# Kernel optimization log

Measured on AMD Instinct MI355X. Metric: run time of the kernel, lower is better.

The kernel has to match this reference:

```python
import jax, jax.numpy as jnp
import numpy as np

B, S, E = 4096, 64, 64   # batch, num fields, embed_dim
A, H = 256, 4            # atten_dim, num_heads
HD = A // H              # head_dim = 64


def setup_inputs() -> dict:
    key = jax.random.key(0)
    ks = jax.random.split(key, 12)
    s = lambda fan_in: 1.0 / np.sqrt(fan_in)
    return {
        "query": jax.random.normal(ks[0], (B, S, E), jnp.float32),
        "key_": jax.random.normal(ks[1], (B, S, E), jnp.float32),
        "value": jax.random.normal(ks[2], (B, S, E), jnp.float32),
        "Wq": jax.random.normal(ks[3], (E, A), jnp.float32) * s(E),
        "bq": jax.random.normal(ks[4], (A,), jnp.float32) * s(E),
        "Wk": jax.random.normal(ks[5], (E, A), jnp.float32) * s(E),
        "bk": jax.random.normal(ks[6], (A,), jnp.float32) * s(E),
        "Wv": jax.random.normal(ks[7], (E, A), jnp.float32) * s(E),
        "bv": jax.random.normal(ks[8], (A,), jnp.float32) * s(E),
        "Wu": jax.random.normal(ks[9], (E, H), jnp.float32) * s(E),
        "bu": jax.random.normal(ks[10], (H,), jnp.float32) * s(E),
        "Wr": jax.random.normal(ks[11], (E, A), jnp.float32) * s(E),
        "br": jnp.zeros((A,), jnp.float32),
    }


def reference(query, key_, value, Wq, bq, Wk, bk, Wv, bv, Wu, bu, Wr, br):
    # Linear projections: [B,S,A]
    q = query @ Wq + bq
    k = key_ @ Wk + bk
    v = value @ Wv + bv
    # Split heads: [B,S,A] -> [B,S,H,HD] -> [H,B,S,HD]
    split = lambda t: t.reshape(B, S, H, HD).transpose(2, 0, 1, 3)
    Q, K, V = split(q), split(k), split(v)
    # Mean-center Q and K over the field (sequence) dimension
    Q = Q - Q.mean(axis=2, keepdims=True)
    K = K - K.mean(axis=2, keepdims=True)
    # Pairwise attention: [H,B,S,S], softmax over keys (no scaling: scale_att=False)
    pairwise = jax.nn.softmax(jnp.einsum('hbqd,hbkd->hbqk', Q, K), axis=-1)
    # Unary term: [B,S,H], softmax over fields, -> [H,B,1,S]
    unary = jax.nn.softmax(key_ @ Wu + bu, axis=1)
    unary = unary.transpose(2, 0, 1)[:, :, None, :]
    attn = pairwise + unary  # dropout p=0 -> identity
    # Weighted values: [H,B,S,HD] -> merge heads -> [B,S,A]
    out = jnp.einsum('hbqk,hbkd->hbqd', attn, V)
    out = out.transpose(1, 2, 0, 3).reshape(B, S, A)
    # Residual branch (W_residual)
    out = out + (query @ Wr + br)
    return out
```

## Files before the change

### kernel.cpp

```cpp
#include <hip/hip_runtime.h>
#include <hip/hip_bf16.h>


#define B_ 4096
#define H_ 4

typedef __attribute__((ext_vector_type(8))) short bf16x8;
typedef __attribute__((ext_vector_type(4))) float f32x4;
typedef __attribute__((ext_vector_type(4))) short s16x4;

#define MFMA16(a, b, c) __builtin_amdgcn_mfma_f32_16x16x32_bf16((a), (b), (c), 0, 0, 0)

static __device__ __forceinline__ short f2b(float f) {
  union { float f; unsigned u; } x; x.f = f;
  unsigned r = x.u + 0x7fffu + ((x.u >> 16) & 1u);
  return (short)(r >> 16);
}
static __device__ __forceinline__ float b2f(short s) {
  union { unsigned u; float f; } x; x.u = ((unsigned)(unsigned short)s) << 16;
  return x.f;
}

#define MTHI 0
#define MTLO 16384
#define WVT  32768
#define WRT  49152
#define WU0  65536

__global__ __launch_bounds__(256)
void prepass(const float* __restrict__ Wq, const float* __restrict__ Wk,
             const float* __restrict__ Wv, const float* __restrict__ Wr,
             const float* __restrict__ Wu, short* __restrict__ ws) {
  int t = blockIdx.x * 256 + threadIdx.x;
  int a = t >> 6, e = t & 63;
  ws[WVT + t] = f2b(Wv[e * 256 + a]);
  ws[WRT + t] = f2b(Wr[e * 256 + a]);
  if (t < 4096) {
    int h = t >> 10, m = (t >> 6) & 15, e2 = t & 63;
    ws[WU0 + t] = (m == 0) ? f2b(Wu[e2 * 4 + h]) : (short)0;
  }
  int h = t >> 12, ep = (t >> 6) & 63;
  const float* wqr = Wq + e * 256 + h * 64;
  const float* wkr = Wk + ep * 256 + h * 64;
  float s = 0.f;
#pragma unroll 8
  for (int aa = 0; aa < 64; ++aa) s += wqr[aa] * wkr[aa];
  short hi = f2b(s);
  ws[MTHI + (h * 64 + ep) * 64 + e] = hi;
  ws[MTLO + (h * 64 + ep) * 64 + e] = f2b(s - b2f(hi));
}

__global__ __launch_bounds__(256, 2)
void attn_main(const float* __restrict__ query, const float* __restrict__ key_,
               const float* __restrict__ value, const float* __restrict__ bv,
               const float* __restrict__ br, const short* __restrict__ ws,
               float* __restrict__ out) {
  const int b    = blockIdx.x;
  const int tid  = threadIdx.x;
  const int w    = tid >> 6;
  const int lane = tid & 63;
  const int quad = lane >> 4;
  const int lc   = lane & 15;
  const int h    = w;

  __shared__ short XqH[64][72];
  __shared__ short XqL[64][72];
  __shared__ short Xk [64][72];
  __shared__ short buf[4][64][72];
  __shared__ float colsq[4][64];
  __shared__ float colsk[4][64];
  __shared__ float mq[64];

  const int crow = w * 16 + (lane >> 2);
  const int cg   = (lane & 3) * 16;
  const float* qp = query + ((size_t)b * 64 + crow) * 64 + cg;
  const float* kp = key_  + ((size_t)b * 64 + crow) * 64 + cg;
  f32x4 qv[4], kv[4];
#pragma unroll
  for (int j = 0; j < 4; ++j) { qv[j] = *(const f32x4*)(qp + 4 * j); kv[j] = *(const f32x4*)(kp + 4 * j); }

  f32x4 sq[4], sk[4];
#pragma unroll
  for (int j = 0; j < 4; ++j) { sq[j] = qv[j]; sk[j] = kv[j]; }
#pragma unroll
  for (int off = 4; off <= 32; off <<= 1)
#pragma unroll
    for (int j = 0; j < 4; ++j)
#pragma unroll
      for (int c = 0; c < 4; ++c) {
        sq[j][c] += __shfl_xor(sq[j][c], off);
        sk[j][c] += __shfl_xor(sk[j][c], off);
      }
  if ((lane & 60) == 0) {
#pragma unroll
    for (int j = 0; j < 4; ++j) {
      *(f32x4*)&colsq[w][cg + 4 * j] = sq[j];
      *(f32x4*)&colsk[w][cg + 4 * j] = sk[j];
    }
  }
  __syncthreads();

  f32x4 mqv[4], mkv[4];
#pragma unroll
  for (int j = 0; j < 4; ++j) {
    f32x4 aq = {0.f, 0.f, 0.f, 0.f}, ak = {0.f, 0.f, 0.f, 0.f};
#pragma unroll
    for (int ww = 0; ww < 4; ++ww) {
      aq += *(const f32x4*)&colsq[ww][cg + 4 * j];
      ak += *(const f32x4*)&colsk[ww][cg + 4 * j];
    }
    mqv[j] = aq * (1.0f / 64.0f);
    mkv[j] = ak * (1.0f / 64.0f);
  }
  if (w == 0 && (lane & 60) == 0)
#pragma unroll
    for (int j = 0; j < 4; ++j) *(f32x4*)&mq[cg + 4 * j] = mqv[j];

#pragma unroll
  for (int half = 0; half < 2; ++half) {
    bf16x8 qh8, ql8, k8;
#pragma unroll
    for (int jj = 0; jj < 8; ++jj) {
      int j = half * 2 + (jj >> 2), c = jj & 3;
      float cq = qv[j][c] - mqv[j][c];
      short hi = f2b(cq);
      qh8[jj] = hi;
      ql8[jj] = f2b(cq - b2f(hi));
      k8[jj]  = f2b(kv[j][c] - mkv[j][c]);
    }
    *(bf16x8*)&XqH[crow][cg + 8 * half] = qh8;
    *(bf16x8*)&XqL[crow][cg + 8 * half] = ql8;
    *(bf16x8*)&Xk [crow][cg + 8 * half] = k8;
  }
  __syncthreads();

  float rho;
  {
    const short* wrr = ws + WRT + (h * 64 + lane) * 64;
    float acc = br[h * 64 + lane];
#pragma unroll
    for (int e8 = 0; e8 < 8; ++e8) {
      bf16x8 w8 = *(const bf16x8*)(wrr + e8 * 8);
#pragma unroll
      for (int j = 0; j < 8; ++j) acc += mq[e8 * 8 + j] * b2f(w8[j]);
    }
    rho = acc;
  }

  bf16x8 xv[4][2];
#pragma unroll
  for (int mt = 0; mt < 4; ++mt)
#pragma unroll
    for (int kk = 0; kk < 2; ++kk) {
      const float* vp = value + ((size_t)b * 64 + mt * 16 + lc) * 64 + kk * 32 + quad * 8;
      f32x4 v0 = *(const f32x4*)vp, v1 = *(const f32x4*)(vp + 4);
#pragma unroll
      for (int j = 0; j < 4; ++j) { xv[mt][kk][j] = f2b(v0[j]); xv[mt][kk][4 + j] = f2b(v1[j]); }
    }

  float usm[4];
  {
    bf16x8 wu[2];
#pragma unroll
    for (int kk = 0; kk < 2; ++kk)
      wu[kk] = *(const bf16x8*)(ws + WU0 + h * 1024 + lc * 64 + kk * 32 + quad * 8);
    f32x4 aU[4];
#pragma unroll
    for (int nt = 0; nt < 4; ++nt) {
      aU[nt] = f32x4{0.f, 0.f, 0.f, 0.f};
#pragma unroll
      for (int kk = 0; kk < 2; ++kk) {
        bf16x8 xb = *(const bf16x8*)&Xk[nt * 16 + lc][kk * 32 + quad * 8];
        aU[nt] = MFMA16(wu[kk], xb, aU[nt]);
      }
    }
    float un[4];
#pragma unroll
    for (int nt = 0; nt < 4; ++nt) un[nt] = __shfl(aU[nt][0], lc);
    float um = fmaxf(fmaxf(un[0], un[1]), fmaxf(un[2], un[3]));
    um = fmaxf(um, __shfl_xor(um, 1)); um = fmaxf(um, __shfl_xor(um, 2));
    um = fmaxf(um, __shfl_xor(um, 4)); um = fmaxf(um, __shfl_xor(um, 8));
    float ue[4], us = 0.f;
#pragma unroll
    for (int nt = 0; nt < 4; ++nt) { ue[nt] = __expf(un[nt] - um); us += ue[nt]; }
    us += __shfl_xor(us, 1); us += __shfl_xor(us, 2);
    us += __shfl_xor(us, 4); us += __shfl_xor(us, 8);
    float uinv = __builtin_amdgcn_rcpf(us);
#pragma unroll
    for (int nt = 0; nt < 4; ++nt) usm[nt] = ue[nt] * uinv;
  }

  {
    bf16x8 mh[4][2], ml[4][2];
#pragma unroll
    for (int nt = 0; nt < 4; ++nt)
#pragma unroll
      for (int kk = 0; kk < 2; ++kk) {
        int off = h * 4096 + (nt * 16 + lc) * 64 + kk * 32 + quad * 8;
        mh[nt][kk] = *(const bf16x8*)(ws + MTHI + off);
        ml[nt][kk] = *(const bf16x8*)(ws + MTLO + off);
      }
    f32x4 aT[4][4];
#pragma unroll
    for (int mt = 0; mt < 4; ++mt) {
      bf16x8 xh[2], xl[2];
#pragma unroll
      for (int kk = 0; kk < 2; ++kk) {
        xh[kk] = *(const bf16x8*)&XqH[mt * 16 + lc][kk * 32 + quad * 8];
        xl[kk] = *(const bf16x8*)&XqL[mt * 16 + lc][kk * 32 + quad * 8];
      }
#pragma unroll
      for (int nt = 0; nt < 4; ++nt) {
        f32x4 acc = {0.f, 0.f, 0.f, 0.f};
#pragma unroll
        for (int kk = 0; kk < 2; ++kk) {
          acc = MFMA16(xh[kk], mh[nt][kk], acc);
          acc = MFMA16(xh[kk], ml[nt][kk], acc);
          acc = MFMA16(xl[kk], mh[nt][kk], acc);
        }
        aT[mt][nt] = acc;
      }
    }
#pragma unroll
    for (int mt = 0; mt < 4; ++mt)
#pragma unroll
      for (int nt = 0; nt < 4; ++nt)
#pragma unroll
        for (int r = 0; r < 4; ++r)
          buf[w][mt * 16 + quad * 4 + r][nt * 16 + lc] = f2b(aT[mt][nt][r]);
  }

  bf16x8 tA[4][2];
#pragma unroll
  for (int mt = 0; mt < 4; ++mt)
#pragma unroll
    for (int kk = 0; kk < 2; ++kk)
      tA[mt][kk] = *(const bf16x8*)&buf[w][mt * 16 + lc][kk * 32 + quad * 8];

#pragma unroll
  for (int mt = 0; mt < 4; ++mt) {
#pragma unroll
    for (int nt = 0; nt < 4; ++nt) {
      f32x4 acc = {0.f, 0.f, 0.f, 0.f};
#pragma unroll
      for (int kk = 0; kk < 2; ++kk) {
        bf16x8 wv8 = *(const bf16x8*)(ws + WVT + (h * 64 + nt * 16 + lc) * 64 + kk * 32 + quad * 8);
        acc = MFMA16(xv[mt][kk], wv8, acc);
      }
      float bvv = bv[h * 64 + nt * 16 + lc];
      s16x4 pk;
#pragma unroll
      for (int r = 0; r < 4; ++r) pk[r] = f2b(acc[r] + bvv);
      *(s16x4*)&buf[w][nt * 16 + lc][mt * 16 + quad * 4] = pk;
    }
  }
  bf16x8 vB[4][2];
#pragma unroll
  for (int nt = 0; nt < 4; ++nt)
#pragma unroll
    for (int kk = 0; kk < 2; ++kk)
      vB[nt][kk] = *(const bf16x8*)&buf[w][nt * 16 + lc][kk * 32 + quad * 8];

  f32x4 aL[4][4];
  {
    bf16x8 xkB[4][2];
#pragma unroll
    for (int nt = 0; nt < 4; ++nt)
#pragma unroll
      for (int kk = 0; kk < 2; ++kk)
        xkB[nt][kk] = *(const bf16x8*)&Xk[nt * 16 + lc][kk * 32 + quad * 8];
#pragma unroll
    for (int mt = 0; mt < 4; ++mt)
#pragma unroll
      for (int nt = 0; nt < 4; ++nt) {
        f32x4 acc = {0.f, 0.f, 0.f, 0.f};
#pragma unroll
        for (int kk = 0; kk < 2; ++kk) acc = MFMA16(tA[mt][kk], xkB[nt][kk], acc);
        aL[mt][nt] = acc;
      }
  }

#pragma unroll
  for (int mt = 0; mt < 4; ++mt)
#pragma unroll
    for (int r = 0; r < 4; ++r) {
      float m = fmaxf(fmaxf(aL[mt][0][r], aL[mt][1][r]), fmaxf(aL[mt][2][r], aL[mt][3][r]));
      m = fmaxf(m, __shfl_xor(m, 1)); m = fmaxf(m, __shfl_xor(m, 2));
      m = fmaxf(m, __shfl_xor(m, 4)); m = fmaxf(m, __shfl_xor(m, 8));
      float e0 = __expf(aL[mt][0][r] - m), e1 = __expf(aL[mt][1][r] - m);
      float e2 = __expf(aL[mt][2][r] - m), e3 = __expf(aL[mt][3][r] - m);
      float s = e0 + e1 + e2 + e3;
      s += __shfl_xor(s, 1); s += __shfl_xor(s, 2);
      s += __shfl_xor(s, 4); s += __shfl_xor(s, 8);
      float inv = __builtin_amdgcn_rcpf(s);
      int row = mt * 16 + quad * 4 + r;
      buf[w][row][lc]      = f2b(e0 * inv + usm[0]);
      buf[w][row][16 + lc] = f2b(e1 * inv + usm[1]);
      buf[w][row][32 + lc] = f2b(e2 * inv + usm[2]);
      buf[w][row][48 + lc] = f2b(e3 * inv + usm[3]);
    }

  bf16x8 pA[4][2];
#pragma unroll
  for (int mt = 0; mt < 4; ++mt)
#pragma unroll
    for (int kk = 0; kk < 2; ++kk)
      pA[mt][kk] = *(const bf16x8*)&buf[w][mt * 16 + lc][kk * 32 + quad * 8];

  float rr[4];
#pragma unroll
  for (int nt = 0; nt < 4; ++nt) rr[nt] = __shfl(rho, nt * 16 + lc);

#pragma unroll
  for (int mt = 0; mt < 4; ++mt) {
    bf16x8 xh[2], xl[2];
#pragma unroll
    for (int kk = 0; kk < 2; ++kk) {
      xh[kk] = *(const bf16x8*)&XqH[mt * 16 + lc][kk * 32 + quad * 8];
      xl[kk] = *(const bf16x8*)&XqL[mt * 16 + lc][kk * 32 + quad * 8];
    }
#pragma unroll
    for (int nt = 0; nt < 4; ++nt) {
      f32x4 acc = {0.f, 0.f, 0.f, 0.f};
#pragma unroll
      for (int kk = 0; kk < 2; ++kk) {
        acc = MFMA16(pA[mt][kk], vB[nt][kk], acc);
        bf16x8 wr8 = *(const bf16x8*)(ws + WRT + (h * 64 + nt * 16 + lc) * 64 + kk * 32 + quad * 8);
        acc = MFMA16(xh[kk], wr8, acc);
        acc = MFMA16(xl[kk], wr8, acc);
      }
      float* op = out + ((size_t)b * 64 + mt * 16 + quad * 4) * 256 + h * 64 + nt * 16 + lc;
#pragma unroll
      for (int r = 0; r < 4; ++r) op[(size_t)r * 256] = acc[r] + rr[nt];
    }
  }
}

extern "C" void kernel_launch(void* const* d_in, const int* in_sizes, int n_in,
                              void* d_out, int out_size, void* d_ws, size_t ws_size,
                              hipStream_t stream) {
  (void)in_sizes; (void)n_in; (void)out_size; (void)ws_size;
  const float* query = (const float*)d_in[0];
  const float* key_  = (const float*)d_in[1];
  const float* value = (const float*)d_in[2];
  const float* Wq    = (const float*)d_in[3];
  const float* Wk    = (const float*)d_in[5];
  const float* Wv    = (const float*)d_in[7];
  const float* bv    = (const float*)d_in[8];
  const float* Wu    = (const float*)d_in[9];
  const float* Wr    = (const float*)d_in[11];
  const float* br    = (const float*)d_in[12];
  short* ws = (short*)d_ws;

  hipLaunchKernelGGL(prepass, dim3(64), dim3(256), 0, stream, Wq, Wk, Wv, Wr, Wu, ws);
  hipLaunchKernelGGL(attn_main, dim3(B_), dim3(256), 0, stream,
                     query, key_, value, bv, br, ws, (float*)d_out);
}
```

Measured before the change: 565.6 us.

## Replace per-wave LDS staging buffer with register shuffles and transposed MFMA operands

```diff
diff --git a/kernel.cpp b/kernel.cpp
--- a/kernel.cpp
+++ b/kernel.cpp
@@ -3,11 +3,9 @@
 
 
 #define B_ 4096
-#define H_ 4
 
 typedef __attribute__((ext_vector_type(8))) short bf16x8;
 typedef __attribute__((ext_vector_type(4))) float f32x4;
-typedef __attribute__((ext_vector_type(4))) short s16x4;
 
 #define MFMA16(a, b, c) __builtin_amdgcn_mfma_f32_16x16x32_bf16((a), (b), (c), 0, 0, 0)
 
@@ -19,6 +17,33 @@
 static __device__ __forceinline__ float b2f(short s) {
   union { unsigned u; float f; } x; x.u = ((unsigned)(unsigned short)s) << 16;
   return x.f;
+}
+static __device__ __forceinline__ unsigned cvtpk(float lo, float hi) {
+  unsigned r;
+  asm volatile("v_cvt_pk_bf16_f32 %0, %1, %2" : "=v"(r) : "v"(lo), "v"(hi));
+  return r;
+}
+
+static __device__ __forceinline__ void qredist(const unsigned pk[4][2], int srcA,
+                                               int srcB, int qhi, bf16x8* fr) {
+  union U { unsigned u[4]; bf16x8 v; };
+#pragma unroll
+  for (int kk = 0; kk < 2; ++kk) {
+    unsigned a0 = (unsigned)__shfl((int)pk[2 * kk][0], srcA);
+    unsigned b0 = (unsigned)__shfl((int)pk[2 * kk + 1][0], srcA);
+    unsigned a1 = (unsigned)__shfl((int)pk[2 * kk][1], srcA);
+    unsigned b1 = (unsigned)__shfl((int)pk[2 * kk + 1][1], srcA);
+    unsigned a2 = (unsigned)__shfl((int)pk[2 * kk][0], srcB);
+    unsigned b2 = (unsigned)__shfl((int)pk[2 * kk + 1][0], srcB);
+    unsigned a3 = (unsigned)__shfl((int)pk[2 * kk][1], srcB);
+    unsigned b3 = (unsigned)__shfl((int)pk[2 * kk + 1][1], srcB);
+    U x;
+    x.u[0] = qhi ? b0 : a0;
+    x.u[1] = qhi ? b1 : a1;
+    x.u[2] = qhi ? b2 : a2;
+    x.u[3] = qhi ? b3 : a3;
+    fr[kk] = x.v;
+  }
 }
 
 #define MTHI 0
@@ -50,7 +75,7 @@
   ws[MTLO + (h * 64 + ep) * 64 + e] = f2b(s - b2f(hi));
 }
 
-__global__ __launch_bounds__(256, 2)
+__global__ __launch_bounds__(256, 3)
 void attn_main(const float* __restrict__ query, const float* __restrict__ key_,
                const float* __restrict__ value, const float* __restrict__ bv,
                const float* __restrict__ br, const short* __restrict__ ws,
@@ -62,11 +87,13 @@
   const int quad = lane >> 4;
   const int lc   = lane & 15;
   const int h    = w;
+  const int qhi  = quad >> 1;
+  const int srcA = lc + 32 * (quad & 1);
+  const int srcB = srcA + 16;
 
   __shared__ short XqH[64][72];
   __shared__ short XqL[64][72];
   __shared__ short Xk [64][72];
-  __shared__ short buf[4][64][72];
   __shared__ float colsq[4][64];
   __shared__ float colsk[4][64];
   __shared__ float mq[64];
@@ -134,6 +161,21 @@
   }
   __syncthreads();
 
+  bf16x8 xv[4][2];
+#pragma unroll
+  for (int mt = 0; mt < 4; ++mt)
+#pragma unroll
+    for (int kk = 0; kk < 2; ++kk) {
+      const float* vp = value + ((size_t)b * 64 + mt * 16 + lc) * 64 + kk * 32 + quad * 8;
+      f32x4 v0 = *(const f32x4*)vp, v1 = *(const f32x4*)(vp + 4);
+      union { unsigned u[4]; bf16x8 v; } pkv;
+      pkv.u[0] = cvtpk(v0[0], v0[1]);
+      pkv.u[1] = cvtpk(v0[2], v0[3]);
+      pkv.u[2] = cvtpk(v1[0], v1[1]);
+      pkv.u[3] = cvtpk(v1[2], v1[3]);
+      xv[mt][kk] = pkv.v;
+    }
+
   float rho;
   {
     const short* wrr = ws + WRT + (h * 64 + lane) * 64;
@@ -146,17 +188,6 @@
     }
     rho = acc;
   }
-
-  bf16x8 xv[4][2];
-#pragma unroll
-  for (int mt = 0; mt < 4; ++mt)
-#pragma unroll
-    for (int kk = 0; kk < 2; ++kk) {
-      const float* vp = value + ((size_t)b * 64 + mt * 16 + lc) * 64 + kk * 32 + quad * 8;
-      f32x4 v0 = *(const f32x4*)vp, v1 = *(const f32x4*)(vp + 4);
-#pragma unroll
-      for (int j = 0; j < 4; ++j) { xv[mt][kk][j] = f2b(v0[j]); xv[mt][kk][4 + j] = f2b(v1[j]); }
-    }
 
   float usm[4];
   {
@@ -190,122 +221,113 @@
     for (int nt = 0; nt < 4; ++nt) usm[nt] = ue[nt] * uinv;
   }
 
-  {
-    bf16x8 mh[4][2], ml[4][2];
-#pragma unroll
-    for (int nt = 0; nt < 4; ++nt)
+  bf16x8 tB[4][2];
+#pragma unroll
+  for (int mtq = 0; mtq < 4; ++mtq) {
+    bf16x8 xqh[2], xql[2];
+#pragma unroll
+    for (int kk = 0; kk < 2; ++kk) {
+      xqh[kk] = *(const bf16x8*)&XqH[mtq * 16 + lc][kk * 32 + quad * 8];
+      xql[kk] = *(const bf16x8*)&XqL[mtq * 16 + lc][kk * 32 + quad * 8];
+    }
+    f32x4 att[4];
+#pragma unroll
+    for (int nt = 0; nt < 4; ++nt) {
+      att[nt] = f32x4{0.f, 0.f, 0.f, 0.f};
 #pragma unroll
       for (int kk = 0; kk < 2; ++kk) {
         int off = h * 4096 + (nt * 16 + lc) * 64 + kk * 32 + quad * 8;
-        mh[nt][kk] = *(const bf16x8*)(ws + MTHI + off);
-        ml[nt][kk] = *(const bf16x8*)(ws + MTLO + off);
+        bf16x8 mh = *(const bf16x8*)(ws + MTHI + off);
+        bf16x8 ml = *(const bf16x8*)(ws + MTLO + off);
+        att[nt] = MFMA16(mh, xqh[kk], att[nt]);
+        att[nt] = MFMA16(ml, xqh[kk], att[nt]);
+        att[nt] = MFMA16(mh, xql[kk], att[nt]);
       }
-    f32x4 aT[4][4];
-#pragma unroll
-    for (int mt = 0; mt < 4; ++mt) {
-      bf16x8 xh[2], xl[2];
-#pragma unroll
-      for (int kk = 0; kk < 2; ++kk) {
-        xh[kk] = *(const bf16x8*)&XqH[mt * 16 + lc][kk * 32 + quad * 8];
-        xl[kk] = *(const bf16x8*)&XqL[mt * 16 + lc][kk * 32 + quad * 8];
-      }
-#pragma unroll
-      for (int nt = 0; nt < 4; ++nt) {
-        f32x4 acc = {0.f, 0.f, 0.f, 0.f};
-#pragma unroll
-        for (int kk = 0; kk < 2; ++kk) {
-          acc = MFMA16(xh[kk], mh[nt][kk], acc);
-          acc = MFMA16(xh[kk], ml[nt][kk], acc);
-          acc = MFMA16(xl[kk], mh[nt][kk], acc);
-        }
-        aT[mt][nt] = acc;
-      }
-    }
-#pragma unroll
-    for (int mt = 0; mt < 4; ++mt)
-#pragma unroll
-      for (int nt = 0; nt < 4; ++nt)
-#pragma unroll
-        for (int r = 0; r < 4; ++r)
-          buf[w][mt * 16 + quad * 4 + r][nt * 16 + lc] = f2b(aT[mt][nt][r]);
-  }
-
-  bf16x8 tA[4][2];
-#pragma unroll
-  for (int mt = 0; mt < 4; ++mt)
+    }
+    unsigned pk[4][2];
+#pragma unroll
+    for (int t = 0; t < 4; ++t) {
+      pk[t][0] = cvtpk(att[t][0], att[t][1]);
+      pk[t][1] = cvtpk(att[t][2], att[t][3]);
+    }
+    qredist(pk, srcA, srcB, qhi, tB[mtq]);
+  }
+
+  f32x4 aLT[4][4];
+#pragma unroll
+  for (int mtk = 0; mtk < 4; ++mtk)
+#pragma unroll
+    for (int mtq = 0; mtq < 4; ++mtq) aLT[mtk][mtq] = f32x4{0.f, 0.f, 0.f, 0.f};
+#pragma unroll
+  for (int mtk = 0; mtk < 4; ++mtk)
+#pragma unroll
+    for (int kk = 0; kk < 2; ++kk) {
+      bf16x8 xkf = *(const bf16x8*)&Xk[mtk * 16 + lc][kk * 32 + quad * 8];
+#pragma unroll
+      for (int mtq = 0; mtq < 4; ++mtq)
+        aLT[mtk][mtq] = MFMA16(xkf, tB[mtq][kk], aLT[mtk][mtq]);
+    }
+
+  float ush[4][4];
+#pragma unroll
+  for (int mtk = 0; mtk < 4; ++mtk)
+#pragma unroll
+    for (int r = 0; r < 4; ++r) ush[mtk][r] = __shfl(usm[mtk], quad * 4 + r);
+
+  bf16x8 pA[4][2];
+#pragma unroll
+  for (int mtq = 0; mtq < 4; ++mtq) {
+    float m = aLT[0][mtq][0];
+#pragma unroll
+    for (int mtk = 0; mtk < 4; ++mtk)
+#pragma unroll
+      for (int r = 0; r < 4; ++r) m = fmaxf(m, aLT[mtk][mtq][r]);
+    m = fmaxf(m, __shfl_xor(m, 16));
+    m = fmaxf(m, __shfl_xor(m, 32));
+    float e[4][4], s = 0.f;
+#pragma unroll
+    for (int mtk = 0; mtk < 4; ++mtk)
+#pragma unroll
+      for (int r = 0; r < 4; ++r) { e[mtk][r] = __expf(aLT[mtk][mtq][r] - m); s += e[mtk][r]; }
+    s += __shfl_xor(s, 16);
+    s += __shfl_xor(s, 32);
+    float inv = __builtin_amdgcn_rcpf(s);
+    unsigned pk[4][2];
+#pragma unroll
+    for (int mtk = 0; mtk < 4; ++mtk) {
+      float p0 = e[mtk][0] * inv + ush[mtk][0];
+      float p1 = e[mtk][1] * inv + ush[mtk][1];
+      float p2 = e[mtk][2] * inv + ush[mtk][2];
+      float p3 = e[mtk][3] * inv + ush[mtk][3];
+      pk[mtk][0] = cvtpk(p0, p1);
+      pk[mtk][1] = cvtpk(p2, p3);
+    }
+    qredist(pk, srcA, srcB, qhi, pA[mtq]);
+  }
+
+  bf16x8 vB[4][2];
+#pragma unroll
+  for (int nt = 0; nt < 4; ++nt) {
+    bf16x8 wv[2];
 #pragma unroll
     for (int kk = 0; kk < 2; ++kk)
-      tA[mt][kk] = *(const bf16x8*)&buf[w][mt * 16 + lc][kk * 32 + quad * 8];
-
-#pragma unroll
-  for (int mt = 0; mt < 4; ++mt) {
-#pragma unroll
-    for (int nt = 0; nt < 4; ++nt) {
-      f32x4 acc = {0.f, 0.f, 0.f, 0.f};
-#pragma unroll
-      for (int kk = 0; kk < 2; ++kk) {
-        bf16x8 wv8 = *(const bf16x8*)(ws + WVT + (h * 64 + nt * 16 + lc) * 64 + kk * 32 + quad * 8);
-        acc = MFMA16(xv[mt][kk], wv8, acc);
-      }
-      float bvv = bv[h * 64 + nt * 16 + lc];
-      s16x4 pk;
-#pragma unroll
-      for (int r = 0; r < 4; ++r) pk[r] = f2b(acc[r] + bvv);
-      *(s16x4*)&buf[w][nt * 16 + lc][mt * 16 + quad * 4] = pk;
-    }
-  }
-  bf16x8 vB[4][2];
-#pragma unroll
-  for (int nt = 0; nt < 4; ++nt)
-#pragma unroll
-    for (int kk = 0; kk < 2; ++kk)
-      vB[nt][kk] = *(const bf16x8*)&buf[w][nt * 16 + lc][kk * 32 + quad * 8];
-
-  f32x4 aL[4][4];
-  {
-    bf16x8 xkB[4][2];
-#pragma unroll
-    for (int nt = 0; nt < 4; ++nt)
-#pragma unroll
-      for (int kk = 0; kk < 2; ++kk)
-        xkB[nt][kk] = *(const bf16x8*)&Xk[nt * 16 + lc][kk * 32 + quad * 8];
-#pragma unroll
-    for (int mt = 0; mt < 4; ++mt)
-#pragma unroll
-      for (int nt = 0; nt < 4; ++nt) {
-        f32x4 acc = {0.f, 0.f, 0.f, 0.f};
-#pragma unroll
-        for (int kk = 0; kk < 2; ++kk) acc = MFMA16(tA[mt][kk], xkB[nt][kk], acc);
-        aL[mt][nt] = acc;
-      }
-  }
-
-#pragma unroll
-  for (int mt = 0; mt < 4; ++mt)
-#pragma unroll
-    for (int r = 0; r < 4; ++r) {
-      float m = fmaxf(fmaxf(aL[mt][0][r], aL[mt][1][r]), fmaxf(aL[mt][2][r], aL[mt][3][r]));
-      m = fmaxf(m, __shfl_xor(m, 1)); m = fmaxf(m, __shfl_xor(m, 2));
-      m = fmaxf(m, __shfl_xor(m, 4)); m = fmaxf(m, __shfl_xor(m, 8));
-      float e0 = __expf(aL[mt][0][r] - m), e1 = __expf(aL[mt][1][r] - m);
-      float e2 = __expf(aL[mt][2][r] - m), e3 = __expf(aL[mt][3][r] - m);
-      float s = e0 + e1 + e2 + e3;
-      s += __shfl_xor(s, 1); s += __shfl_xor(s, 2);
-      s += __shfl_xor(s, 4); s += __shfl_xor(s, 8);
-      float inv = __builtin_amdgcn_rcpf(s);
-      int row = mt * 16 + quad * 4 + r;
-      buf[w][row][lc]      = f2b(e0 * inv + usm[0]);
-      buf[w][row][16 + lc] = f2b(e1 * inv + usm[1]);
-      buf[w][row][32 + lc] = f2b(e2 * inv + usm[2]);
-      buf[w][row][48 + lc] = f2b(e3 * inv + usm[3]);
-    }
-
-  bf16x8 pA[4][2];
-#pragma unroll
-  for (int mt = 0; mt < 4; ++mt)
-#pragma unroll
-    for (int kk = 0; kk < 2; ++kk)
-      pA[mt][kk] = *(const bf16x8*)&buf[w][mt * 16 + lc][kk * 32 + quad * 8];
+      wv[kk] = *(const bf16x8*)(ws + WVT + (h * 64 + nt * 16 + lc) * 64 + kk * 32 + quad * 8);
+    f32x4 av[4];
+#pragma unroll
+    for (int mtk = 0; mtk < 4; ++mtk) {
+      av[mtk] = f32x4{0.f, 0.f, 0.f, 0.f};
+#pragma unroll
+      for (int kk = 0; kk < 2; ++kk) av[mtk] = MFMA16(xv[mtk][kk], wv[kk], av[mtk]);
+    }
+    float bvv = bv[h * 64 + nt * 16 + lc];
+    unsigned pk[4][2];
+#pragma unroll
+    for (int mtk = 0; mtk < 4; ++mtk) {
+      pk[mtk][0] = cvtpk(av[mtk][0] + bvv, av[mtk][1] + bvv);
+      pk[mtk][1] = cvtpk(av[mtk][2] + bvv, av[mtk][3] + bvv);
+    }
+    qredist(pk, srcA, srcB, qhi, vB[nt]);
+  }
 
   float rr[4];
 #pragma unroll
```

Result: slower. 649.3 us (+14.8%).

## Split attention work across 16 waves per block, one per head and row tile

Applied to the files above, without the earlier changes.

```diff
diff --git a/kernel.cpp b/kernel.cpp
--- a/kernel.cpp
+++ b/kernel.cpp
@@ -3,7 +3,6 @@
 
 
 #define B_ 4096
-#define H_ 4
 
 typedef __attribute__((ext_vector_type(8))) short bf16x8;
 typedef __attribute__((ext_vector_type(4))) float f32x4;
@@ -50,7 +49,7 @@
   ws[MTLO + (h * 64 + ep) * 64 + e] = f2b(s - b2f(hi));
 }
 
-__global__ __launch_bounds__(256, 2)
+__global__ __launch_bounds__(1024, 4)
 void attn_main(const float* __restrict__ query, const float* __restrict__ key_,
                const float* __restrict__ value, const float* __restrict__ bv,
                const float* __restrict__ br, const short* __restrict__ ws,
@@ -61,78 +60,75 @@
   const int lane = tid & 63;
   const int quad = lane >> 4;
   const int lc   = lane & 15;
-  const int h    = w;
+  const int h    = w >> 2;
+  const int mt   = w & 3;
 
   __shared__ short XqH[64][72];
   __shared__ short XqL[64][72];
   __shared__ short Xk [64][72];
-  __shared__ short buf[4][64][72];
-  __shared__ float colsq[4][64];
-  __shared__ float colsk[4][64];
+  __shared__ short Tbuf [4][64][72];
+  __shared__ short VTbuf[4][64][72];
+  __shared__ float colsq[16][64];
+  __shared__ float colsk[16][64];
   __shared__ float mq[64];
 
-  const int crow = w * 16 + (lane >> 2);
-  const int cg   = (lane & 3) * 16;
-  const float* qp = query + ((size_t)b * 64 + crow) * 64 + cg;
-  const float* kp = key_  + ((size_t)b * 64 + crow) * 64 + cg;
-  f32x4 qv[4], kv[4];
-#pragma unroll
-  for (int j = 0; j < 4; ++j) { qv[j] = *(const f32x4*)(qp + 4 * j); kv[j] = *(const f32x4*)(kp + 4 * j); }
-
-  f32x4 sq[4], sk[4];
-#pragma unroll
-  for (int j = 0; j < 4; ++j) { sq[j] = qv[j]; sk[j] = kv[j]; }
-#pragma unroll
-  for (int off = 4; off <= 32; off <<= 1)
-#pragma unroll
-    for (int j = 0; j < 4; ++j)
-#pragma unroll
-      for (int c = 0; c < 4; ++c) {
-        sq[j][c] += __shfl_xor(sq[j][c], off);
-        sk[j][c] += __shfl_xor(sk[j][c], off);
-      }
-  if ((lane & 60) == 0) {
-#pragma unroll
-    for (int j = 0; j < 4; ++j) {
-      *(f32x4*)&colsq[w][cg + 4 * j] = sq[j];
-      *(f32x4*)&colsk[w][cg + 4 * j] = sk[j];
-    }
+  const int row = tid >> 4;
+  const int c0  = (tid & 15) * 4;
+  const float* qp = query + ((size_t)b * 64 + row) * 64 + c0;
+  const float* kp = key_  + ((size_t)b * 64 + row) * 64 + c0;
+  f32x4 qv = *(const f32x4*)qp;
+  f32x4 kv = *(const f32x4*)kp;
+
+  const float* vp = value + ((size_t)b * 64 + mt * 16 + lc) * 64 + quad * 8;
+  f32x4 va0 = *(const f32x4*)(vp);
+  f32x4 va1 = *(const f32x4*)(vp + 4);
+  f32x4 vb0 = *(const f32x4*)(vp + 32);
+  f32x4 vb1 = *(const f32x4*)(vp + 36);
+
+  f32x4 sq = qv, sk = kv;
+#pragma unroll
+  for (int c = 0; c < 4; ++c) {
+    sq[c] += __shfl_xor(sq[c], 16); sk[c] += __shfl_xor(sk[c], 16);
+    sq[c] += __shfl_xor(sq[c], 32); sk[c] += __shfl_xor(sk[c], 32);
+  }
+  if (lane < 16) {
+    *(f32x4*)&colsq[w][c0] = sq;
+    *(f32x4*)&colsk[w][c0] = sk;
   }
   __syncthreads();
 
-  f32x4 mqv[4], mkv[4];
+  f32x4 aq = {0.f, 0.f, 0.f, 0.f}, ak = {0.f, 0.f, 0.f, 0.f};
+#pragma unroll
+  for (int ww = 0; ww < 16; ++ww) {
+    aq += *(const f32x4*)&colsq[ww][c0];
+    ak += *(const f32x4*)&colsk[ww][c0];
+  }
+  f32x4 mqv = aq * (1.0f / 64.0f);
+  f32x4 mkv = ak * (1.0f / 64.0f);
+  if (tid < 16) *(f32x4*)&mq[c0] = mqv;
+
+  {
+    s16x4 qh4, ql4, k4;
+#pragma unroll
+    for (int c = 0; c < 4; ++c) {
+      float cq = qv[c] - mqv[c];
+      short hi = f2b(cq);
+      qh4[c] = hi;
+      ql4[c] = f2b(cq - b2f(hi));
+      k4[c]  = f2b(kv[c] - mkv[c]);
+    }
+    *(s16x4*)&XqH[row][c0] = qh4;
+    *(s16x4*)&XqL[row][c0] = ql4;
+    *(s16x4*)&Xk [row][c0] = k4;
+  }
+  __syncthreads();
+
+  bf16x8 xv[2];
 #pragma unroll
   for (int j = 0; j < 4; ++j) {
-    f32x4 aq = {0.f, 0.f, 0.f, 0.f}, ak = {0.f, 0.f, 0.f, 0.f};
-#pragma unroll
-    for (int ww = 0; ww < 4; ++ww) {
-      aq += *(const f32x4*)&colsq[ww][cg + 4 * j];
-      ak += *(const f32x4*)&colsk[ww][cg + 4 * j];
-    }
-    mqv[j] = aq * (1.0f / 64.0f);
-    mkv[j] = ak * (1.0f / 64.0f);
-  }
-  if (w == 0 && (lane & 60) == 0)
-#pragma unroll
-    for (int j = 0; j < 4; ++j) *(f32x4*)&mq[cg + 4 * j] = mqv[j];
-
-#pragma unroll
-  for (int half = 0; half < 2; ++half) {
-    bf16x8 qh8, ql8, k8;
-#pragma unroll
-    for (int jj = 0; jj < 8; ++jj) {
-      int j = half * 2 + (jj >> 2), c = jj & 3;
-      float cq = qv[j][c] - mqv[j][c];
-      short hi = f2b(cq);
-      qh8[jj] = hi;
-      ql8[jj] = f2b(cq - b2f(hi));
-      k8[jj]  = f2b(kv[j][c] - mkv[j][c]);
-    }
-    *(bf16x8*)&XqH[crow][cg + 8 * half] = qh8;
-    *(bf16x8*)&XqL[crow][cg + 8 * half] = ql8;
-    *(bf16x8*)&Xk [crow][cg + 8 * half] = k8;
-  }
-  __syncthreads();
+    xv[0][j] = f2b(va0[j]); xv[0][4 + j] = f2b(va1[j]);
+    xv[1][j] = f2b(vb0[j]); xv[1][4 + j] = f2b(vb1[j]);
+  }
 
   float rho;
   {
@@ -146,17 +142,6 @@
     }
     rho = acc;
   }
-
-  bf16x8 xv[4][2];
-#pragma unroll
-  for (int mt = 0; mt < 4; ++mt)
-#pragma unroll
-    for (int kk = 0; kk < 2; ++kk) {
-      const float* vp = value + ((size_t)b * 64 + mt * 16 + lc) * 64 + kk * 32 + quad * 8;
-      f32x4 v0 = *(const f32x4*)vp, v1 = *(const f32x4*)(vp + 4);
-#pragma unroll
-      for (int j = 0; j < 4; ++j) { xv[mt][kk][j] = f2b(v0[j]); xv[mt][kk][4 + j] = f2b(v1[j]); }
-    }
 
   float usm[4];
   {
@@ -190,149 +175,116 @@
     for (int nt = 0; nt < 4; ++nt) usm[nt] = ue[nt] * uinv;
   }
 
+  bf16x8 xh[2], xl[2];
+#pragma unroll
+  for (int kk = 0; kk < 2; ++kk) {
+    xh[kk] = *(const bf16x8*)&XqH[mt * 16 + lc][kk * 32 + quad * 8];
+    xl[kk] = *(const bf16x8*)&XqL[mt * 16 + lc][kk * 32 + quad * 8];
+  }
   {
-    bf16x8 mh[4][2], ml[4][2];
-#pragma unroll
-    for (int nt = 0; nt < 4; ++nt)
+    f32x4 aT[4];
+#pragma unroll
+    for (int nt = 0; nt < 4; ++nt) {
+      f32x4 acc = {0.f, 0.f, 0.f, 0.f};
 #pragma unroll
       for (int kk = 0; kk < 2; ++kk) {
         int off = h * 4096 + (nt * 16 + lc) * 64 + kk * 32 + quad * 8;
-        mh[nt][kk] = *(const bf16x8*)(ws + MTHI + off);
-        ml[nt][kk] = *(const bf16x8*)(ws + MTLO + off);
+        bf16x8 mh = *(const bf16x8*)(ws + MTHI + off);
+        bf16x8 ml = *(const bf16x8*)(ws + MTLO + off);
+        acc = MFMA16(xh[kk], mh, acc);
+        acc = MFMA16(xh[kk], ml, acc);
+        acc = MFMA16(xl[kk], mh, acc);
       }
-    f32x4 aT[4][4];
-#pragma unroll
-    for (int mt = 0; mt < 4; ++mt) {
-      bf16x8 xh[2], xl[2];
-#pragma unroll
-      for (int kk = 0; kk < 2; ++kk) {
-        xh[kk] = *(const bf16x8*)&XqH[mt * 16 + lc][kk * 32 + quad * 8];
-        xl[kk] = *(const bf16x8*)&XqL[mt * 16 + lc][kk * 32 + quad * 8];
-      }
-#pragma unroll
-      for (int nt = 0; nt < 4; ++nt) {
-        f32x4 acc = {0.f, 0.f, 0.f, 0.f};
-#pragma unroll
-        for (int kk = 0; kk < 2; ++kk) {
-          acc = MFMA16(xh[kk], mh[nt][kk], acc);
-          acc = MFMA16(xh[kk], ml[nt][kk], acc);
-          acc = MFMA16(xl[kk], mh[nt][kk], acc);
-        }
-        aT[mt][nt] = acc;
-      }
-    }
-#pragma unroll
-    for (int mt = 0; mt < 4; ++mt)
-#pragma unroll
-      for (int nt = 0; nt < 4; ++nt)
-#pragma unroll
-        for (int r = 0; r < 4; ++r)
-          buf[w][mt * 16 + quad * 4 + r][nt * 16 + lc] = f2b(aT[mt][nt][r]);
-  }
-
-  bf16x8 tA[4][2];
-#pragma unroll
-  for (int mt = 0; mt < 4; ++mt)
+      aT[nt] = acc;
+    }
+#pragma unroll
+    for (int nt = 0; nt < 4; ++nt)
+#pragma unroll
+      for (int r = 0; r < 4; ++r)
+        Tbuf[h][mt * 16 + quad * 4 + r][nt * 16 + lc] = f2b(aT[nt][r]);
+  }
+
+  bf16x8 tA[2];
+#pragma unroll
+  for (int kk = 0; kk < 2; ++kk)
+    tA[kk] = *(const bf16x8*)&Tbuf[h][mt * 16 + lc][kk * 32 + quad * 8];
+
+#pragma unroll
+  for (int nt = 0; nt < 4; ++nt) {
+    f32x4 acc = {0.f, 0.f, 0.f, 0.f};
+#pragma unroll
+    for (int kk = 0; kk < 2; ++kk) {
+      bf16x8 wv8 = *(const bf16x8*)(ws + WVT + (h * 64 + nt * 16 + lc) * 64 + kk * 32 + quad * 8);
+      acc = MFMA16(xv[kk], wv8, acc);
+    }
+    float bvv = bv[h * 64 + nt * 16 + lc];
+    s16x4 pk;
+#pragma unroll
+    for (int r = 0; r < 4; ++r) pk[r] = f2b(acc[r] + bvv);
+    *(s16x4*)&VTbuf[h][nt * 16 + lc][mt * 16 + quad * 4] = pk;
+  }
+
+  f32x4 aL[4];
+#pragma unroll
+  for (int nt = 0; nt < 4; ++nt) {
+    f32x4 acc = {0.f, 0.f, 0.f, 0.f};
+#pragma unroll
+    for (int kk = 0; kk < 2; ++kk) {
+      bf16x8 xkB = *(const bf16x8*)&Xk[nt * 16 + lc][kk * 32 + quad * 8];
+      acc = MFMA16(tA[kk], xkB, acc);
+    }
+    aL[nt] = acc;
+  }
+
+#pragma unroll
+  for (int r = 0; r < 4; ++r) {
+    float m = fmaxf(fmaxf(aL[0][r], aL[1][r]), fmaxf(aL[2][r], aL[3][r]));
+    m = fmaxf(m, __shfl_xor(m, 1)); m = fmaxf(m, __shfl_xor(m, 2));
+    m = fmaxf(m, __shfl_xor(m, 4)); m = fmaxf(m, __shfl_xor(m, 8));
+    float e0 = __expf(aL[0][r] - m), e1 = __expf(aL[1][r] - m);
+    float e2 = __expf(aL[2][r] - m), e3 = __expf(aL[3][r] - m);
+    float s = e0 + e1 + e2 + e3;
+    s += __shfl_xor(s, 1); s += __shfl_xor(s, 2);
+    s += __shfl_xor(s, 4); s += __shfl_xor(s, 8);
+    float inv = __builtin_amdgcn_rcpf(s);
+    int rw = mt * 16 + quad * 4 + r;
+    Tbuf[h][rw][lc]      = f2b(e0 * inv + usm[0]);
+    Tbuf[h][rw][16 + lc] = f2b(e1 * inv + usm[1]);
+    Tbuf[h][rw][32 + lc] = f2b(e2 * inv + usm[2]);
+    Tbuf[h][rw][48 + lc] = f2b(e3 * inv + usm[3]);
+  }
+
+  bf16x8 pA[2];
+#pragma unroll
+  for (int kk = 0; kk < 2; ++kk)
+    pA[kk] = *(const bf16x8*)&Tbuf[h][mt * 16 + lc][kk * 32 + quad * 8];
+
+  float rr[4];
+#pragma unroll
+  for (int nt = 0; nt < 4; ++nt) rr[nt] = __shfl(rho, nt * 16 + lc);
+
+  __syncthreads();
+
+  bf16x8 vB[4][2];
+#pragma unroll
+  for (int nt = 0; nt < 4; ++nt)
 #pragma unroll
     for (int kk = 0; kk < 2; ++kk)
-      tA[mt][kk] = *(const bf16x8*)&buf[w][mt * 16 + lc][kk * 32 + quad * 8];
-
-#pragma unroll
-  for (int mt = 0; mt < 4; ++mt) {
-#pragma unroll
-    for (int nt = 0; nt < 4; ++nt) {
-      f32x4 acc = {0.f, 0.f, 0.f, 0.f};
-#pragma unroll
-      for (int kk = 0; kk < 2; ++kk) {
-        bf16x8 wv8 = *(const bf16x8*)(ws + WVT + (h * 64 + nt * 16 + lc) * 64 + kk * 32 + quad * 8);
-        acc = MFMA16(xv[mt][kk], wv8, acc);
-      }
-      float bvv = bv[h * 64 + nt * 16 + lc];
-      s16x4 pk;
-#pragma unroll
-      for (int r = 0; r < 4; ++r) pk[r] = f2b(acc[r] + bvv);
-      *(s16x4*)&buf[w][nt * 16 + lc][mt * 16 + quad * 4] = pk;
-    }
-  }
-  bf16x8 vB[4][2];
-#pragma unroll
-  for (int nt = 0; nt < 4; ++nt)
-#pragma unroll
-    for (int kk = 0; kk < 2; ++kk)
-      vB[nt][kk] = *(const bf16x8*)&buf[w][nt * 16 + lc][kk * 32 + quad * 8];
-
-  f32x4 aL[4][4];
-  {
-    bf16x8 xkB[4][2];
-#pragma unroll
-    for (int nt = 0; nt < 4; ++nt)
-#pragma unroll
-      for (int kk = 0; kk < 2; ++kk)
-        xkB[nt][kk] = *(const bf16x8*)&Xk[nt * 16 + lc][kk * 32 + quad * 8];
-#pragma unroll
-    for (int mt = 0; mt < 4; ++mt)
-#pragma unroll
-      for (int nt = 0; nt < 4; ++nt) {
-        f32x4 acc = {0.f, 0.f, 0.f, 0.f};
-#pragma unroll
-        for (int kk = 0; kk < 2; ++kk) acc = MFMA16(tA[mt][kk], xkB[nt][kk], acc);
-        aL[mt][nt] = acc;
-      }
-  }
-
-#pragma unroll
-  for (int mt = 0; mt < 4; ++mt)
-#pragma unroll
-    for (int r = 0; r < 4; ++r) {
-      float m = fmaxf(fmaxf(aL[mt][0][r], aL[mt][1][r]), fmaxf(aL[mt][2][r], aL[mt][3][r]));
-      m = fmaxf(m, __shfl_xor(m, 1)); m = fmaxf(m, __shfl_xor(m, 2));
-      m = fmaxf(m, __shfl_xor(m, 4)); m = fmaxf(m, __shfl_xor(m, 8));
-      float e0 = __expf(aL[mt][0][r] - m), e1 = __expf(aL[mt][1][r] - m);
-      float e2 = __expf(aL[mt][2][r] - m), e3 = __expf(aL[mt][3][r] - m);
-      float s = e0 + e1 + e2 + e3;
-      s += __shfl_xor(s, 1); s += __shfl_xor(s, 2);
-      s += __shfl_xor(s, 4); s += __shfl_xor(s, 8);
-      float inv = __builtin_amdgcn_rcpf(s);
-      int row = mt * 16 + quad * 4 + r;
-      buf[w][row][lc]      = f2b(e0 * inv + usm[0]);
-      buf[w][row][16 + lc] = f2b(e1 * inv + usm[1]);
-      buf[w][row][32 + lc] = f2b(e2 * inv + usm[2]);
-      buf[w][row][48 + lc] = f2b(e3 * inv + usm[3]);
-    }
-
-  bf16x8 pA[4][2];
-#pragma unroll
-  for (int mt = 0; mt < 4; ++mt)
-#pragma unroll
-    for (int kk = 0; kk < 2; ++kk)
-      pA[mt][kk] = *(const bf16x8*)&buf[w][mt * 16 + lc][kk * 32 + quad * 8];
-
-  float rr[4];
-#pragma unroll
-  for (int nt = 0; nt < 4; ++nt) rr[nt] = __shfl(rho, nt * 16 + lc);
-
-#pragma unroll
-  for (int mt = 0; mt < 4; ++mt) {
-    bf16x8 xh[2], xl[2];
+      vB[nt][kk] = *(const bf16x8*)&VTbuf[h][nt * 16 + lc][kk * 32 + quad * 8];
+
+#pragma unroll
+  for (int nt = 0; nt < 4; ++nt) {
+    f32x4 acc = {0.f, 0.f, 0.f, 0.f};
 #pragma unroll
     for (int kk = 0; kk < 2; ++kk) {
-      xh[kk] = *(const bf16x8*)&XqH[mt * 16 + lc][kk * 32 + quad * 8];
-      xl[kk] = *(const bf16x8*)&XqL[mt * 16 + lc][kk * 32 + quad * 8];
-    }
-#pragma unroll
-    for (int nt = 0; nt < 4; ++nt) {
-      f32x4 acc = {0.f, 0.f, 0.f, 0.f};
-#pragma unroll
-      for (int kk = 0; kk < 2; ++kk) {
-        acc = MFMA16(pA[mt][kk], vB[nt][kk], acc);
-        bf16x8 wr8 = *(const bf16x8*)(ws + WRT + (h * 64 + nt * 16 + lc) * 64 + kk * 32 + quad * 8);
-        acc = MFMA16(xh[kk], wr8, acc);
-        acc = MFMA16(xl[kk], wr8, acc);
-      }
-      float* op = out + ((size_t)b * 64 + mt * 16 + quad * 4) * 256 + h * 64 + nt * 16 + lc;
-#pragma unroll
-      for (int r = 0; r < 4; ++r) op[(size_t)r * 256] = acc[r] + rr[nt];
-    }
+      acc = MFMA16(pA[kk], vB[nt][kk], acc);
+      bf16x8 wr8 = *(const bf16x8*)(ws + WRT + (h * 64 + nt * 16 + lc) * 64 + kk * 32 + quad * 8);
+      acc = MFMA16(xh[kk], wr8, acc);
+      acc = MFMA16(xl[kk], wr8, acc);
+    }
+    float* op = out + ((size_t)b * 64 + mt * 16 + quad * 4) * 256 + h * 64 + nt * 16 + lc;
+#pragma unroll
+    for (int r = 0; r < 4; ++r) op[(size_t)r * 256] = acc[r] + rr[nt];
   }
 }
 
@@ -353,6 +305,6 @@
   short* ws = (short*)d_ws;
 
   hipLaunchKernelGGL(prepass, dim3(64), dim3(256), 0, stream, Wq, Wk, Wv, Wr, Wu, ws);
-  hipLaunchKernelGGL(attn_main, dim3(B_), dim3(256), 0, stream,
+  hipLaunchKernelGGL(attn_main, dim3(B_), dim3(1024), 0, stream,
                      query, key_, value, bv, br, ws, (float*)d_out);
 }
```

New measurement: 762.3 us. 34.8% more time.

## Reassociate value projection after attention and process query tiles one at a time

Applied to the files above, without the earlier changes.

```diff
diff --git a/kernel.cpp b/kernel.cpp
--- a/kernel.cpp
+++ b/kernel.cpp
@@ -3,7 +3,6 @@
 
 
 #define B_ 4096
-#define H_ 4
 
 typedef __attribute__((ext_vector_type(8))) short bf16x8;
 typedef __attribute__((ext_vector_type(4))) float f32x4;
@@ -19,6 +18,11 @@
 static __device__ __forceinline__ float b2f(short s) {
   union { unsigned u; float f; } x; x.u = ((unsigned)(unsigned short)s) << 16;
   return x.f;
+}
+static __device__ __forceinline__ unsigned cvtpk(float lo, float hi) {
+  unsigned r;
+  asm volatile("v_cvt_pk_bf16_f32 %0, %1, %2" : "=v"(r) : "v"(lo), "v"(hi));
+  return r;
 }
 
 #define MTHI 0
@@ -50,7 +54,7 @@
   ws[MTLO + (h * 64 + ep) * 64 + e] = f2b(s - b2f(hi));
 }
 
-__global__ __launch_bounds__(256, 2)
+__global__ __launch_bounds__(256, 4)
 void attn_main(const float* __restrict__ query, const float* __restrict__ key_,
                const float* __restrict__ value, const float* __restrict__ bv,
                const float* __restrict__ br, const short* __restrict__ ws,
@@ -66,10 +70,10 @@
   __shared__ short XqH[64][72];
   __shared__ short XqL[64][72];
   __shared__ short Xk [64][72];
-  __shared__ short buf[4][64][72];
-  __shared__ float colsq[4][64];
-  __shared__ float colsk[4][64];
+  __shared__ short buf[4][16][72];
   __shared__ float mq[64];
+  float* colsq = (float*)&buf[0][0][0];
+  float* colsk = colsq + 256;
 
   const int crow = w * 16 + (lane >> 2);
   const int cg   = (lane & 3) * 16;
@@ -79,6 +83,18 @@
 #pragma unroll
   for (int j = 0; j < 4; ++j) { qv[j] = *(const f32x4*)(qp + 4 * j); kv[j] = *(const f32x4*)(kp + 4 * j); }
 
+  float xvf[4][2][8];
+  {
+    const float* vbase = value + (size_t)b * 4096 + quad * 512 + lc;
+#pragma unroll
+    for (int nt = 0; nt < 4; ++nt)
+#pragma unroll
+      for (int kk = 0; kk < 2; ++kk)
+#pragma unroll
+        for (int j = 0; j < 8; ++j)
+          xvf[nt][kk][j] = vbase[(kk * 32 + j) * 64 + nt * 16];
+  }
+
   f32x4 sq[4], sk[4];
 #pragma unroll
   for (int j = 0; j < 4; ++j) { sq[j] = qv[j]; sk[j] = kv[j]; }
@@ -94,8 +110,8 @@
   if ((lane & 60) == 0) {
 #pragma unroll
     for (int j = 0; j < 4; ++j) {
-      *(f32x4*)&colsq[w][cg + 4 * j] = sq[j];
-      *(f32x4*)&colsk[w][cg + 4 * j] = sk[j];
+      *(f32x4*)&colsq[w * 64 + cg + 4 * j] = sq[j];
+      *(f32x4*)&colsk[w * 64 + cg + 4 * j] = sk[j];
     }
   }
   __syncthreads();
@@ -106,8 +122,8 @@
     f32x4 aq = {0.f, 0.f, 0.f, 0.f}, ak = {0.f, 0.f, 0.f, 0.f};
 #pragma unroll
     for (int ww = 0; ww < 4; ++ww) {
-      aq += *(const f32x4*)&colsq[ww][cg + 4 * j];
-      ak += *(const f32x4*)&colsk[ww][cg + 4 * j];
+      aq += *(const f32x4*)&colsq[ww * 64 + cg + 4 * j];
+      ak += *(const f32x4*)&colsk[ww * 64 + cg + 4 * j];
     }
     mqv[j] = aq * (1.0f / 64.0f);
     mkv[j] = ak * (1.0f / 64.0f);
@@ -132,12 +148,24 @@
     *(bf16x8*)&XqL[crow][cg + 8 * half] = ql8;
     *(bf16x8*)&Xk [crow][cg + 8 * half] = k8;
   }
+
+  bf16x8 xvB[4][2];
+#pragma unroll
+  for (int nt = 0; nt < 4; ++nt)
+#pragma unroll
+    for (int kk = 0; kk < 2; ++kk) {
+      union { unsigned u[4]; bf16x8 v; } pk;
+#pragma unroll
+      for (int p = 0; p < 4; ++p)
+        pk.u[p] = cvtpk(xvf[nt][kk][2 * p], xvf[nt][kk][2 * p + 1]);
+      xvB[nt][kk] = pk.v;
+    }
   __syncthreads();
 
   float rho;
   {
     const short* wrr = ws + WRT + (h * 64 + lane) * 64;
-    float acc = br[h * 64 + lane];
+    float acc = br[h * 64 + lane] + 2.0f * bv[h * 64 + lane];
 #pragma unroll
     for (int e8 = 0; e8 < 8; ++e8) {
       bf16x8 w8 = *(const bf16x8*)(wrr + e8 * 8);
@@ -146,17 +174,9 @@
     }
     rho = acc;
   }
-
-  bf16x8 xv[4][2];
-#pragma unroll
-  for (int mt = 0; mt < 4; ++mt)
-#pragma unroll
-    for (int kk = 0; kk < 2; ++kk) {
-      const float* vp = value + ((size_t)b * 64 + mt * 16 + lc) * 64 + kk * 32 + quad * 8;
-      f32x4 v0 = *(const f32x4*)vp, v1 = *(const f32x4*)(vp + 4);
-#pragma unroll
-      for (int j = 0; j < 4; ++j) { xv[mt][kk][j] = f2b(v0[j]); xv[mt][kk][4 + j] = f2b(v1[j]); }
-    }
+  float rr[4];
+#pragma unroll
+  for (int nt = 0; nt < 4; ++nt) rr[nt] = __shfl(rho, nt * 16 + lc);
 
   float usm[4];
   {
@@ -190,141 +210,101 @@
     for (int nt = 0; nt < 4; ++nt) usm[nt] = ue[nt] * uinv;
   }
 
-  {
-    bf16x8 mh[4][2], ml[4][2];
-#pragma unroll
-    for (int nt = 0; nt < 4; ++nt)
-#pragma unroll
-      for (int kk = 0; kk < 2; ++kk) {
-        int off = h * 4096 + (nt * 16 + lc) * 64 + kk * 32 + quad * 8;
-        mh[nt][kk] = *(const bf16x8*)(ws + MTHI + off);
-        ml[nt][kk] = *(const bf16x8*)(ws + MTLO + off);
-      }
-    f32x4 aT[4][4];
-#pragma unroll
-    for (int mt = 0; mt < 4; ++mt) {
-      bf16x8 xh[2], xl[2];
-#pragma unroll
-      for (int kk = 0; kk < 2; ++kk) {
-        xh[kk] = *(const bf16x8*)&XqH[mt * 16 + lc][kk * 32 + quad * 8];
-        xl[kk] = *(const bf16x8*)&XqL[mt * 16 + lc][kk * 32 + quad * 8];
-      }
+  for (int mt = 0; mt < 4; ++mt) {
+    bf16x8 xh[2], xl[2];
+#pragma unroll
+    for (int kk = 0; kk < 2; ++kk) {
+      xh[kk] = *(const bf16x8*)&XqH[mt * 16 + lc][kk * 32 + quad * 8];
+      xl[kk] = *(const bf16x8*)&XqL[mt * 16 + lc][kk * 32 + quad * 8];
+    }
+
+    {
+      f32x4 aT[4];
 #pragma unroll
       for (int nt = 0; nt < 4; ++nt) {
         f32x4 acc = {0.f, 0.f, 0.f, 0.f};
 #pragma unroll
         for (int kk = 0; kk < 2; ++kk) {
-          acc = MFMA16(xh[kk], mh[nt][kk], acc);
-          acc = MFMA16(xh[kk], ml[nt][kk], acc);
-          acc = MFMA16(xl[kk], mh[nt][kk], acc);
+          int off = h * 4096 + (nt * 16 + lc) * 64 + kk * 32 + quad * 8;
+          bf16x8 mh = *(const bf16x8*)(ws + MTHI + off);
+          bf16x8 ml = *(const bf16x8*)(ws + MTLO + off);
+          acc = MFMA16(xh[kk], mh, acc);
+          acc = MFMA16(xh[kk], ml, acc);
+          acc = MFMA16(xl[kk], mh, acc);
         }
-        aT[mt][nt] = acc;
-      }
-    }
-#pragma unroll
-    for (int mt = 0; mt < 4; ++mt)
+        aT[nt] = acc;
+      }
 #pragma unroll
       for (int nt = 0; nt < 4; ++nt)
 #pragma unroll
         for (int r = 0; r < 4; ++r)
-          buf[w][mt * 16 + quad * 4 + r][nt * 16 + lc] = f2b(aT[mt][nt][r]);
-  }
-
-  bf16x8 tA[4][2];
-#pragma unroll
-  for (int mt = 0; mt < 4; ++mt)
+          buf[w][quad * 4 + r][nt * 16 + lc] = f2b(aT[nt][r]);
+    }
+    bf16x8 tA[2];
 #pragma unroll
     for (int kk = 0; kk < 2; ++kk)
-      tA[mt][kk] = *(const bf16x8*)&buf[w][mt * 16 + lc][kk * 32 + quad * 8];
-
-#pragma unroll
-  for (int mt = 0; mt < 4; ++mt) {
+      tA[kk] = *(const bf16x8*)&buf[w][lc][kk * 32 + quad * 8];
+
+    f32x4 aL[4];
 #pragma unroll
     for (int nt = 0; nt < 4; ++nt) {
       f32x4 acc = {0.f, 0.f, 0.f, 0.f};
 #pragma unroll
       for (int kk = 0; kk < 2; ++kk) {
-        bf16x8 wv8 = *(const bf16x8*)(ws + WVT + (h * 64 + nt * 16 + lc) * 64 + kk * 32 + quad * 8);
-        acc = MFMA16(xv[mt][kk], wv8, acc);
-      }
-      float bvv = bv[h * 64 + nt * 16 + lc];
-      s16x4 pk;
-#pragma unroll
-      for (int r = 0; r < 4; ++r) pk[r] = f2b(acc[r] + bvv);
-      *(s16x4*)&buf[w][nt * 16 + lc][mt * 16 + quad * 4] = pk;
-    }
-  }
-  bf16x8 vB[4][2];
-#pragma unroll
-  for (int nt = 0; nt < 4; ++nt)
-#pragma unroll
-    for (int kk = 0; kk < 2; ++kk)
-      vB[nt][kk] = *(const bf16x8*)&buf[w][nt * 16 + lc][kk * 32 + quad * 8];
-
-  f32x4 aL[4][4];
-  {
-    bf16x8 xkB[4][2];
-#pragma unroll
-    for (int nt = 0; nt < 4; ++nt)
-#pragma unroll
-      for (int kk = 0; kk < 2; ++kk)
-        xkB[nt][kk] = *(const bf16x8*)&Xk[nt * 16 + lc][kk * 32 + quad * 8];
-#pragma unroll
-    for (int mt = 0; mt < 4; ++mt)
-#pragma unroll
-      for (int nt = 0; nt < 4; ++nt) {
-        f32x4 acc = {0.f, 0.f, 0.f, 0.f};
-#pragma unroll
-        for (int kk = 0; kk < 2; ++kk) acc = MFMA16(tA[mt][kk], xkB[nt][kk], acc);
-        aL[mt][nt] = acc;
-      }
-  }
-
-#pragma unroll
-  for (int mt = 0; mt < 4; ++mt)
+        bf16x8 xkB = *(const bf16x8*)&Xk[nt * 16 + lc][kk * 32 + quad * 8];
+        acc = MFMA16(tA[kk], xkB, acc);
+      }
+      aL[nt] = acc;
+    }
+
 #pragma unroll
     for (int r = 0; r < 4; ++r) {
-      float m = fmaxf(fmaxf(aL[mt][0][r], aL[mt][1][r]), fmaxf(aL[mt][2][r], aL[mt][3][r]));
+      float m = fmaxf(fmaxf(aL[0][r], aL[1][r]), fmaxf(aL[2][r], aL[3][r]));
       m = fmaxf(m, __shfl_xor(m, 1)); m = fmaxf(m, __shfl_xor(m, 2));
       m = fmaxf(m, __shfl_xor(m, 4)); m = fmaxf(m, __shfl_xor(m, 8));
-      float e0 = __expf(aL[mt][0][r] - m), e1 = __expf(aL[mt][1][r] - m);
-      float e2 = __expf(aL[mt][2][r] - m), e3 = __expf(aL[mt][3][r] - m);
+      float e0 = __expf(aL[0][r] - m), e1 = __expf(aL[1][r] - m);
+      float e2 = __expf(aL[2][r] - m), e3 = __expf(aL[3][r] - m);
       float s = e0 + e1 + e2 + e3;
       s += __shfl_xor(s, 1); s += __shfl_xor(s, 2);
       s += __shfl_xor(s, 4); s += __shfl_xor(s, 8);
       float inv = __builtin_amdgcn_rcpf(s);
-      int row = mt * 16 + quad * 4 + r;
-      buf[w][row][lc]      = f2b(e0 * inv + usm[0]);
-      buf[w][row][16 + lc] = f2b(e1 * inv + usm[1]);
-      buf[w][row][32 + lc] = f2b(e2 * inv + usm[2]);
-      buf[w][row][48 + lc] = f2b(e3 * inv + usm[3]);
-    }
-
-  bf16x8 pA[4][2];
-#pragma unroll
-  for (int mt = 0; mt < 4; ++mt)
+      buf[w][quad * 4 + r][lc]      = f2b(e0 * inv + usm[0]);
+      buf[w][quad * 4 + r][16 + lc] = f2b(e1 * inv + usm[1]);
+      buf[w][quad * 4 + r][32 + lc] = f2b(e2 * inv + usm[2]);
+      buf[w][quad * 4 + r][48 + lc] = f2b(e3 * inv + usm[3]);
+    }
+    bf16x8 pA[2];
 #pragma unroll
     for (int kk = 0; kk < 2; ++kk)
-      pA[mt][kk] = *(const bf16x8*)&buf[w][mt * 16 + lc][kk * 32 + quad * 8];
-
-  float rr[4];
-#pragma unroll
-  for (int nt = 0; nt < 4; ++nt) rr[nt] = __shfl(rho, nt * 16 + lc);
-
-#pragma unroll
-  for (int mt = 0; mt < 4; ++mt) {
-    bf16x8 xh[2], xl[2];
-#pragma unroll
-    for (int kk = 0; kk < 2; ++kk) {
-      xh[kk] = *(const bf16x8*)&XqH[mt * 16 + lc][kk * 32 + quad * 8];
-      xl[kk] = *(const bf16x8*)&XqL[mt * 16 + lc][kk * 32 + quad * 8];
-    }
+      pA[kk] = *(const bf16x8*)&buf[w][lc][kk * 32 + quad * 8];
+
+    {
+      f32x4 aG[4];
+#pragma unroll
+      for (int nt = 0; nt < 4; ++nt) {
+        f32x4 acc = {0.f, 0.f, 0.f, 0.f};
+#pragma unroll
+        for (int kk = 0; kk < 2; ++kk) acc = MFMA16(pA[kk], xvB[nt][kk], acc);
+        aG[nt] = acc;
+      }
+#pragma unroll
+      for (int nt = 0; nt < 4; ++nt)
+#pragma unroll
+        for (int r = 0; r < 4; ++r)
+          buf[w][quad * 4 + r][nt * 16 + lc] = f2b(aG[nt][r]);
+    }
+    bf16x8 gA[2];
+#pragma unroll
+    for (int kk = 0; kk < 2; ++kk)
+      gA[kk] = *(const bf16x8*)&buf[w][lc][kk * 32 + quad * 8];
+
 #pragma unroll
     for (int nt = 0; nt < 4; ++nt) {
       f32x4 acc = {0.f, 0.f, 0.f, 0.f};
 #pragma unroll
       for (int kk = 0; kk < 2; ++kk) {
-        acc = MFMA16(pA[mt][kk], vB[nt][kk], acc);
+        bf16x8 wv8 = *(const bf16x8*)(ws + WVT + (h * 64 + nt * 16 + lc) * 64 + kk * 32 + quad * 8);
+        acc = MFMA16(gA[kk], wv8, acc);
         bf16x8 wr8 = *(const bf16x8*)(ws + WRT + (h * 64 + nt * 16 + lc) * 64 + kk * 32 + quad * 8);
         acc = MFMA16(xh[kk], wr8, acc);
         acc = MFMA16(xl[kk], wr8, acc);
```

New measurement: 976.8 us. 1.73x slower.
